# Kernel tuning notes

Hardware: AMD Instinct MI355X
Metric: run time of the kernel (lower is better)

Reference implementation:

```python
import jax, jax.numpy as jnp
import numpy as np

B, S, DIN, DOUT, A, T, H = 8, 1024, 1024, 1024, 4, 4, 8  # arity A, T cell types, hidden H


def setup_inputs() -> dict:
    key = jax.random.key(0)
    ks = jax.random.split(key, 6)
    x = jax.random.normal(ks[0], (B, S, DIN), jnp.float32)
    sc = 1.0 / np.sqrt(DIN).astype(np.float32)
    weight = jax.random.uniform(ks[1], (A * DOUT, DIN), jnp.float32, -sc, sc)
    bias = jax.random.uniform(ks[2], (A * DOUT,), jnp.float32, -sc, sc)
    # stacked per-cell-type MLP params: arity -> H -> 1 (tanh)
    cw1 = jax.random.normal(ks[3], (T, A, H), jnp.float32) / np.sqrt(A).astype(np.float32)
    cb1 = jnp.zeros((T, H), jnp.float32)
    cw2 = jax.random.normal(ks[4], (T, H), jnp.float32) / np.sqrt(H).astype(np.float32)
    cb2 = jnp.zeros((T,), jnp.float32)
    return {"x": x, "weight": weight, "bias": bias,
            "cw1": cw1, "cb1": cb1, "cw2": cw2, "cb2": cb2}


def reference(x, weight, bias, cw1, cb1, cw2, cb2):
    T_, A_, H_ = cw1.shape
    Dout = weight.shape[0] // A_
    G = Dout // T_  # neurons per cell type (cell_indices = contiguous blocks via np.repeat)
    # all_inputs = F.linear(input, weight, bias): (B, S, A*Dout)
    z = jnp.einsum('bsd,od->bso', x, weight) + bias
    # slice per-neuron arity chunks -> (B, S, T, G, A)
    z = z.reshape(z.shape[0], z.shape[1], T_, G, A_)
    # per-cell-type MLP applied to every neuron of that type (replaces Python loop)
    h = jnp.tanh(jnp.einsum('bstga,tah->bstgh', z, cw1) + cb1[:, None, :])
    o = jnp.einsum('bstgh,th->bstg', h, cw2) + cb2[:, None]
    # concat over neurons -> (B, S, Dout)
    return o.reshape(o.shape[0], o.shape[1], Dout)
```

## Files before the change

kernel.cpp:

```cpp
#include <hip/hip_runtime.h>


typedef __bf16 bf16x8 __attribute__((ext_vector_type(8)));
typedef float f32x4 __attribute__((ext_vector_type(4)));
typedef float f32x16 __attribute__((ext_vector_type(16)));

#define BM 256
#define BN 128
#define BK 32
#define KDIM 1024
#define NT 32
#define ABUF 16384
#define BUFB 24576
#define ZSTRIDE 132
#define XN8 (8192 * 1024 / 8)
#define WN8 (4096 * 1024 / 8)

__global__ __launch_bounds__(256) void cvt_bf16_kernel(
    const float* __restrict__ x, const float* __restrict__ w,
    __bf16* __restrict__ xb, __bf16* __restrict__ wb) {
    int i = blockIdx.x * 256 + threadIdx.x;
    const float* src;
    __bf16* dst;
    int j;
    if (i < XN8) { src = x; dst = xb; j = i; }
    else         { src = w; dst = wb; j = i - XN8; }
    const f32x4* p = (const f32x4*)src + 2 * (size_t)j;
    f32x4 a = p[0], b = p[1];
    bf16x8 o;
    o[0] = (__bf16)a[0]; o[1] = (__bf16)a[1]; o[2] = (__bf16)a[2]; o[3] = (__bf16)a[3];
    o[4] = (__bf16)b[0]; o[5] = (__bf16)b[1]; o[6] = (__bf16)b[2]; o[7] = (__bf16)b[3];
    ((bf16x8*)dst)[j] = o;
}

union __align__(16) SmemU {
    unsigned char raw[2 * BUFB];
    float z[64 * ZSTRIDE];
};

__global__ __launch_bounds__(256, 2) void fused_gemm_mlp_kernel(
    const __bf16* __restrict__ Ag,
    const __bf16* __restrict__ Bg,
    const float* __restrict__ bias,
    const float* __restrict__ cw1,
    const float* __restrict__ cb1,
    const float* __restrict__ cw2,
    const float* __restrict__ cb2,
    float* __restrict__ out)
{
    __shared__ SmemU u;

    const int tid  = threadIdx.x;
    const int wave = tid >> 6;
    const int lane = tid & 63;
    const int wm = wave >> 1;
    const int wn = wave & 1;
    const int bn0 = blockIdx.x * BN;
    const int bm0 = blockIdx.y * BM;

    f32x16 acc[4][2] = {};

    const int qloc = lane >> 3;
    const int slog = (lane & 7) ^ qloc;
    const int arow = 2 * qloc + (slog >> 2);
    const int acol = (slog & 3) * 8;

    const int lr5 = lane & 31;
    const int lk2 = lane >> 5;
    const int lrh = lr5 >> 1;
    const int lp  = lr5 & 1;
    int a_addr[2], b_addr[2];
#pragma unroll
    for (int kh = 0; kh < 2; ++kh) {
        const int slot = (((lp * 4) + (kh * 2 + lk2)) ^ (lrh & 7)) * 16;
        a_addr[kh] = wm * 8192 + lrh * 128 + slot;
        b_addr[kh] = ABUF + wn * 4096 + lrh * 128 + slot;
    }
    const char* sb = (const char*)u.raw;

    auto stage = [&](int t) {
        const int bb = (t & 1) * BUFB;
        const int k0 = t * BK;
#pragma unroll
        for (int c = 0; c < 4; ++c) {
            const int ch = wave + c * 4;
            const __bf16* g = Ag + (size_t)(bm0 + ch * 16 + arow) * KDIM + k0 + acol;
            __builtin_amdgcn_global_load_lds(
                (__attribute__((address_space(1))) void*)g,
                (__attribute__((address_space(3))) void*)&u.raw[bb + ch * 1024],
                16, 0, 0);
        }
#pragma unroll
        for (int c = 0; c < 2; ++c) {
            const int ch = wave + c * 4;
            const __bf16* g = Bg + (size_t)(bn0 + ch * 16 + arow) * KDIM + k0 + acol;
            __builtin_amdgcn_global_load_lds(
                (__attribute__((address_space(1))) void*)g,
                (__attribute__((address_space(3))) void*)&u.raw[bb + ABUF + ch * 1024],
                16, 0, 0);
        }
    };

    stage(0);
    __syncthreads();

    for (int t = 0; t < NT; ++t) {
        if (t + 1 < NT) stage(t + 1);

        const int cb = (t & 1) * BUFB;
#pragma unroll
        for (int kh = 0; kh < 2; ++kh) {
            bf16x8 af[4], bfr[2];
#pragma unroll
            for (int mi = 0; mi < 4; ++mi)
                af[mi] = *(const bf16x8*)(sb + cb + a_addr[kh] + mi * 2048);
#pragma unroll
            for (int ni = 0; ni < 2; ++ni)
                bfr[ni] = *(const bf16x8*)(sb + cb + b_addr[kh] + ni * 2048);
#pragma unroll
            for (int mi = 0; mi < 4; ++mi)
#pragma unroll
                for (int ni = 0; ni < 2; ++ni)
                    acc[mi][ni] = __builtin_amdgcn_mfma_f32_32x32x16_bf16(
                        af[mi], bfr[ni], acc[mi][ni], 0, 0, 0);
        }
        __syncthreads();
    }

    const int t = bn0 >> 10;
    float w1[32], b1[8], w2[8];
#pragma unroll
    for (int i = 0; i < 32; ++i) w1[i] = cw1[t * 32 + i];
#pragma unroll
    for (int i = 0; i < 8; ++i) { b1[i] = cb1[t * 8 + i]; w2[i] = cw2[t * 8 + i]; }
    const float b2 = cb2[t];

    float bcol[2];
#pragma unroll
    for (int ni = 0; ni < 2; ++ni)
        bcol[ni] = bias[bn0 + wn * 64 + ni * 32 + lr5];

    const float L2E2 = 2.885390081777927f;

#pragma unroll
    for (int h = 0; h < 4; ++h) {
        if (wm == (h >> 1)) {
            const int mi0 = (h & 1) * 2;
#pragma unroll
            for (int dmi = 0; dmi < 2; ++dmi) {
                const int mi = mi0 + dmi;
#pragma unroll
                for (int ni = 0; ni < 2; ++ni) {
                    const int n = wn * 64 + ni * 32 + lr5;
#pragma unroll
                    for (int g = 0; g < 4; ++g) {
                        const int rb = dmi * 32 + g * 8 + lk2 * 4;
                        u.z[(rb + 0) * ZSTRIDE + n] = acc[mi][ni][g * 4 + 0] + bcol[ni];
                        u.z[(rb + 1) * ZSTRIDE + n] = acc[mi][ni][g * 4 + 1] + bcol[ni];
                        u.z[(rb + 2) * ZSTRIDE + n] = acc[mi][ni][g * 4 + 2] + bcol[ni];
                        u.z[(rb + 3) * ZSTRIDE + n] = acc[mi][ni][g * 4 + 3] + bcol[ni];
                    }
                }
            }
        }
        __syncthreads();

#pragma unroll
        for (int it = 0; it < 8; ++it) {
            const int i = tid + it * 256;
            const int q = i & 31;
            const int r = i >> 5;
            f32x4 z = *(const f32x4*)&u.z[r * ZSTRIDE + 4 * q];
            float o = 0.f;
#pragma unroll
            for (int hh = 0; hh < 8; ++hh) {
                float pre = z[0] * w1[0 * 8 + hh] + z[1] * w1[1 * 8 + hh]
                          + z[2] * w1[2 * 8 + hh] + z[3] * w1[3 * 8 + hh] + b1[hh];
                float e = __builtin_amdgcn_exp2f(pre * L2E2);
                float th = 1.0f - 2.0f * __builtin_amdgcn_rcpf(e + 1.0f);
                o += th * w2[hh];
            }
            o += b2;
            out[(size_t)(bm0 + h * 64 + r) * 1024 + (bn0 >> 2) + q] = o;
        }
        __syncthreads();
    }
}

extern "C" void kernel_launch(void* const* d_in, const int* in_sizes, int n_in,
                              void* d_out, int out_size, void* d_ws, size_t ws_size,
                              hipStream_t stream) {
    const float* x    = (const float*)d_in[0];
    const float* w    = (const float*)d_in[1];
    const float* bias = (const float*)d_in[2];
    const float* cw1  = (const float*)d_in[3];
    const float* cb1  = (const float*)d_in[4];
    const float* cw2  = (const float*)d_in[5];
    const float* cb2  = (const float*)d_in[6];
    float* out = (float*)d_out;

    __bf16* xb = (__bf16*)d_ws;
    __bf16* wb = xb + (size_t)8192 * 1024;

    cvt_bf16_kernel<<<(XN8 + WN8) / 256, 256, 0, stream>>>(x, w, xb, wb);

    dim3 grid(4096 / BN, 8192 / BM);
    fused_gemm_mlp_kernel<<<grid, 256, 0, stream>>>(xb, wb, bias, cw1, cb1, cw2, cb2, out);
}
```

Before: 192.0 us.

## Permute weight rows at conversion so MLP epilogue runs in registers

The bf16 conversion kernel now writes weight rows in a permuted order. Within each 128-column tile, the four arity inputs of a neuron then fall into four separate 32-column MFMA sub-tiles at the same lane position. The GEMM warp layout becomes 4x1 (each wave covers 64 rows by all 128 columns), so each lane holds all four arity values for its neuron. That lets the per-neuron MLP be computed directly from the accumulators, removing the LDS staging of z and the extra barriers in the epilogue. The trade-off is a different fragment-reuse ratio (2 A by 4 B loads per wave) and strided output stores.

```diff
diff --git a/kernel.cpp b/kernel.cpp
--- a/kernel.cpp
+++ b/kernel.cpp
@@ -12,7 +12,6 @@
 #define NT 32
 #define ABUF 16384
 #define BUFB 24576
-#define ZSTRIDE 132
 #define XN8 (8192 * 1024 / 8)
 #define WN8 (4096 * 1024 / 8)
 
@@ -22,21 +21,24 @@
     int i = blockIdx.x * 256 + threadIdx.x;
     const float* src;
     __bf16* dst;
-    int j;
-    if (i < XN8) { src = x; dst = xb; j = i; }
-    else         { src = w; dst = wb; j = i - XN8; }
+    int j, jdst;
+    if (i < XN8) { src = x; dst = xb; j = i; jdst = i; }
+    else {
+        src = w; dst = wb; j = i - XN8;
+        const int r  = j >> 7;
+        const int c8 = j & 127;
+        const int q  = r >> 2;
+        const int a  = r & 3;
+        const int rn = ((q >> 5) << 7) + (a << 5) + (q & 31);
+        jdst = (rn << 7) + c8;
+    }
     const f32x4* p = (const f32x4*)src + 2 * (size_t)j;
     f32x4 a = p[0], b = p[1];
     bf16x8 o;
     o[0] = (__bf16)a[0]; o[1] = (__bf16)a[1]; o[2] = (__bf16)a[2]; o[3] = (__bf16)a[3];
     o[4] = (__bf16)b[0]; o[5] = (__bf16)b[1]; o[6] = (__bf16)b[2]; o[7] = (__bf16)b[3];
-    ((bf16x8*)dst)[j] = o;
+    ((bf16x8*)dst)[jdst] = o;
 }
-
-union __align__(16) SmemU {
-    unsigned char raw[2 * BUFB];
-    float z[64 * ZSTRIDE];
-};
 
 __global__ __launch_bounds__(256, 2) void fused_gemm_mlp_kernel(
     const __bf16* __restrict__ Ag,
@@ -48,17 +50,16 @@
     const float* __restrict__ cb2,
     float* __restrict__ out)
 {
-    __shared__ SmemU u;
+    __shared__ __align__(16) unsigned char raw[2 * BUFB];
 
     const int tid  = threadIdx.x;
     const int wave = tid >> 6;
     const int lane = tid & 63;
-    const int wm = wave >> 1;
-    const int wn = wave & 1;
+    const int wm = wave;
     const int bn0 = blockIdx.x * BN;
     const int bm0 = blockIdx.y * BM;
 
-    f32x16 acc[4][2] = {};
+    f32x16 acc[2][4] = {};
 
     const int qloc = lane >> 3;
     const int slog = (lane & 7) ^ qloc;
@@ -73,10 +74,10 @@
 #pragma unroll
     for (int kh = 0; kh < 2; ++kh) {
         const int slot = (((lp * 4) + (kh * 2 + lk2)) ^ (lrh & 7)) * 16;
-        a_addr[kh] = wm * 8192 + lrh * 128 + slot;
-        b_addr[kh] = ABUF + wn * 4096 + lrh * 128 + slot;
+        a_addr[kh] = wm * 4096 + lrh * 128 + slot;
+        b_addr[kh] = ABUF + lrh * 128 + slot;
     }
-    const char* sb = (const char*)u.raw;
+    const char* sb = (const char*)raw;
 
     auto stage = [&](int t) {
         const int bb = (t & 1) * BUFB;
@@ -87,7 +88,7 @@
             const __bf16* g = Ag + (size_t)(bm0 + ch * 16 + arow) * KDIM + k0 + acol;
             __builtin_amdgcn_global_load_lds(
                 (__attribute__((address_space(1))) void*)g,
-                (__attribute__((address_space(3))) void*)&u.raw[bb + ch * 1024],
+                (__attribute__((address_space(3))) void*)&raw[bb + ch * 1024],
                 16, 0, 0);
         }
 #pragma unroll
@@ -96,7 +97,7 @@
             const __bf16* g = Bg + (size_t)(bn0 + ch * 16 + arow) * KDIM + k0 + acol;
             __builtin_amdgcn_global_load_lds(
                 (__attribute__((address_space(1))) void*)g,
-                (__attribute__((address_space(3))) void*)&u.raw[bb + ABUF + ch * 1024],
+                (__attribute__((address_space(3))) void*)&raw[bb + ABUF + ch * 1024],
                 16, 0, 0);
         }
     };
@@ -110,80 +111,57 @@
         const int cb = (t & 1) * BUFB;
 #pragma unroll
         for (int kh = 0; kh < 2; ++kh) {
-            bf16x8 af[4], bfr[2];
+            bf16x8 af[2], bfr[4];
 #pragma unroll
-            for (int mi = 0; mi < 4; ++mi)
+            for (int mi = 0; mi < 2; ++mi)
                 af[mi] = *(const bf16x8*)(sb + cb + a_addr[kh] + mi * 2048);
 #pragma unroll
-            for (int ni = 0; ni < 2; ++ni)
-                bfr[ni] = *(const bf16x8*)(sb + cb + b_addr[kh] + ni * 2048);
+            for (int a = 0; a < 4; ++a)
+                bfr[a] = *(const bf16x8*)(sb + cb + b_addr[kh] + a * 2048);
 #pragma unroll
-            for (int mi = 0; mi < 4; ++mi)
+            for (int mi = 0; mi < 2; ++mi)
 #pragma unroll
-                for (int ni = 0; ni < 2; ++ni)
-                    acc[mi][ni] = __builtin_amdgcn_mfma_f32_32x32x16_bf16(
-                        af[mi], bfr[ni], acc[mi][ni], 0, 0, 0);
+                for (int a = 0; a < 4; ++a)
+                    acc[mi][a] = __builtin_amdgcn_mfma_f32_32x32x16_bf16(
+                        af[mi], bfr[a], acc[mi][a], 0, 0, 0);
         }
         __syncthreads();
     }
 
-    const int t = bn0 >> 10;
+    const int tct = bn0 >> 10;
     float w1[32], b1[8], w2[8];
 #pragma unroll
-    for (int i = 0; i < 32; ++i) w1[i] = cw1[t * 32 + i];
+    for (int i = 0; i < 32; ++i) w1[i] = cw1[tct * 32 + i];
 #pragma unroll
-    for (int i = 0; i < 8; ++i) { b1[i] = cb1[t * 8 + i]; w2[i] = cw2[t * 8 + i]; }
-    const float b2 = cb2[t];
+    for (int i = 0; i < 8; ++i) { b1[i] = cb1[tct * 8 + i]; w2[i] = cw2[tct * 8 + i]; }
+    const float b2 = cb2[tct];
 
-    float bcol[2];
-#pragma unroll
-    for (int ni = 0; ni < 2; ++ni)
-        bcol[ni] = bias[bn0 + wn * 64 + ni * 32 + lr5];
+    const f32x4 bz = *(const f32x4*)&bias[bn0 + 4 * lr5];
 
     const float L2E2 = 2.885390081777927f;
+    float* outp = out + (size_t)(bm0 + wm * 64 + 4 * lk2) * 1024 + (bn0 >> 2) + lr5;
 
 #pragma unroll
-    for (int h = 0; h < 4; ++h) {
-        if (wm == (h >> 1)) {
-            const int mi0 = (h & 1) * 2;
+    for (int mi = 0; mi < 2; ++mi) {
 #pragma unroll
-            for (int dmi = 0; dmi < 2; ++dmi) {
-                const int mi = mi0 + dmi;
-#pragma unroll
-                for (int ni = 0; ni < 2; ++ni) {
-                    const int n = wn * 64 + ni * 32 + lr5;
-#pragma unroll
-                    for (int g = 0; g < 4; ++g) {
-                        const int rb = dmi * 32 + g * 8 + lk2 * 4;
-                        u.z[(rb + 0) * ZSTRIDE + n] = acc[mi][ni][g * 4 + 0] + bcol[ni];
-                        u.z[(rb + 1) * ZSTRIDE + n] = acc[mi][ni][g * 4 + 1] + bcol[ni];
-                        u.z[(rb + 2) * ZSTRIDE + n] = acc[mi][ni][g * 4 + 2] + bcol[ni];
-                        u.z[(rb + 3) * ZSTRIDE + n] = acc[mi][ni][g * 4 + 3] + bcol[ni];
-                    }
-                }
-            }
-        }
-        __syncthreads();
-
-#pragma unroll
-        for (int it = 0; it < 8; ++it) {
-            const int i = tid + it * 256;
-            const int q = i & 31;
-            const int r = i >> 5;
-            f32x4 z = *(const f32x4*)&u.z[r * ZSTRIDE + 4 * q];
+        for (int g = 0; g < 16; ++g) {
+            const float z0 = acc[mi][0][g] + bz[0];
+            const float z1 = acc[mi][1][g] + bz[1];
+            const float z2 = acc[mi][2][g] + bz[2];
+            const float z3 = acc[mi][3][g] + bz[3];
             float o = 0.f;
 #pragma unroll
             for (int hh = 0; hh < 8; ++hh) {
-                float pre = z[0] * w1[0 * 8 + hh] + z[1] * w1[1 * 8 + hh]
-                          + z[2] * w1[2 * 8 + hh] + z[3] * w1[3 * 8 + hh] + b1[hh];
+                float pre = z0 * w1[0 * 8 + hh] + z1 * w1[1 * 8 + hh]
+                          + z2 * w1[2 * 8 + hh] + z3 * w1[3 * 8 + hh] + b1[hh];
                 float e = __builtin_amdgcn_exp2f(pre * L2E2);
                 float th = 1.0f - 2.0f * __builtin_amdgcn_rcpf(e + 1.0f);
                 o += th * w2[hh];
             }
             o += b2;
-            out[(size_t)(bm0 + h * 64 + r) * 1024 + (bn0 >> 2) + q] = o;
+            const int row = mi * 32 + (g & 3) + 8 * (g >> 2);
+            outp[(size_t)row * 1024] = o;
         }
-        __syncthreads();
     }
 }
 
```

New measurement: 190.5 us (median of 2 runs). Within noise of the previous version (-0.8%).
